# Optimization experiments

Hardware: AMD Instinct MI355X
Metric: run time of the kernel (lower is better)

## Reference

```python
import jax, jax.numpy as jnp
import numpy as np
import math

NUM_SEGMENTS = 4      # num_bezier_segments
SHARPNESS = 75.0
SAMPLE_RATE = 16      # curve samples per bezier segment


def _control_radians(S):
    # replicates the __init__ control-polygon angle construction
    theta = math.pi * 2 / (4 * S) + math.atan(math.tan(2 * math.pi / (4 * S)) / 3.0)
    r = []
    for i in range(S):
        base = 2 * math.pi / S * i
        r += [base, base + theta, 2 * math.pi / S * (i + 1) - theta]
    return jnp.asarray(np.asarray(r, dtype=np.float32).reshape(S, 3))


def _quat_rotate_inv(q, p):
    # rotate p (...,3) by the conjugate of quaternion q (...,4), wxyz convention
    q = q / jnp.linalg.norm(q, axis=-1, keepdims=True)
    w = q[..., 0:1]
    v = -q[..., 1:4]
    t = 2.0 * jnp.cross(v, p)
    return p + w * t + jnp.cross(v, t)


def _csg_stump(points, primitive_parameters, iw, uw, is_training):
    pp = jnp.swapaxes(primitive_parameters, 1, 2)          # (B,K,P)
    B, K, P = pp.shape
    S, R = NUM_SEGMENTS, SAMPLE_RATE
    quat = pp[:, :, :4]
    trans = pp[:, :, 4:7]
    height = pp[:, :, 7]                                   # (B,K)
    radius = jnp.abs(pp[:, :, 8:8 + 3 * S].reshape(B, K, S, 3))
    wts = jnp.abs(pp[:, :, 8 + 3 * S:8 + 5 * S].reshape(B, K, S, 2))

    rad = _control_radians(S)                              # (S,3)
    cp = jnp.stack([jnp.cos(rad) * radius, jnp.sin(rad) * radius], axis=-1)  # (B,K,S,3,2)

    # closed rational cubic bezier spline: segment s uses cp[s,0..2] and cp[s+1,0]
    P0, P1, P2 = cp[:, :, :, 0], cp[:, :, :, 1], cp[:, :, :, 2]
    P3 = jnp.roll(P0, -1, axis=2)
    t = jnp.arange(R, dtype=pp.dtype) / R                  # (R,) endpoint-free
    b0 = (1 - t) ** 3; b1 = 3 * t * (1 - t) ** 2; b2 = 3 * t ** 2 * (1 - t); b3 = t ** 3
    w1 = wts[..., 0:1]; w2 = wts[..., 1:2]                 # (B,K,S,1)
    num = (b0[:, None] * P0[..., None, :]
           + (b1[:, None] * w1[..., None]) * P1[..., None, :]
           + (b2[:, None] * w2[..., None]) * P2[..., None, :]
           + b3[:, None] * P3[..., None, :])               # (B,K,S,R,2)
    den = b0 + b1 * w1 + b2 * w2 + b3                       # (B,K,S,R)
    curve = (num / den[..., None]).reshape(B, K, S * R, 2)  # (B,K,N,2)

    # transform query points into each primitive's local frame
    p_loc = _quat_rotate_inv(quat[:, None], points[:, :, None, :] - trans[:, None])  # (B,M,K,3)
    pxy = p_loc[..., :2]
    pz = p_loc[..., 2]

    # point-to-curve distances without materializing the (B,M,K,N,2) diff
    p_sq = jnp.sum(pxy * pxy, axis=-1)                      # (B,M,K)
    c_sq = jnp.sum(curve * curve, axis=-1)                  # (B,K,N)
    dots = jnp.einsum('bmkd,bknd->bmkn', pxy, curve)
    d = jnp.sqrt(jnp.maximum(p_sq[..., None] + c_sq[:, None] - 2.0 * dots, 0.0) + 1e-12)
    ud = jnp.min(d, axis=-1)                                # (B,M,K) unsigned 2D distance
    idx = jnp.argmin(d, axis=-1)
    curve_r = jnp.sqrt(c_sq)                                # (B,K,N)
    r_near = jnp.take_along_axis(jnp.broadcast_to(curve_r[:, None], d.shape),
                                 idx[..., None], axis=-1)[..., 0]
    sign = jax.lax.stop_gradient(jnp.where(jnp.sqrt(p_sq) <= r_near, -1.0, 1.0))
    sdf2d = sign * ud

    # extrusion along z
    dz = jnp.abs(pz) - height[:, None, :]
    primitive_sdf = (jnp.minimum(jnp.maximum(sdf2d, dz), 0.0)
                     + jnp.sqrt(jnp.maximum(sdf2d, 0.0) ** 2 + jnp.maximum(dz, 0.0) ** 2 + 1e-12))
    support_distances = ud

    occ = jax.nn.sigmoid(-primitive_sdf * SHARPNESS)        # (B,M,K)

    # soft intersection: bkc,bmk->bmkc selection
    pre_i = iw[:, None] * occ[..., None] + (1.0 - iw)[:, None]    # (B,M,K,C)
    if is_training:
        w = jax.lax.stop_gradient(jax.nn.softmax(pre_i * -40.0, axis=-2))
        inter = jnp.sum(w * pre_i, axis=-2)                 # (B,M,C)
    else:
        inter = jnp.min(pre_i, axis=-2)

    # soft union
    pre_u = uw[:, None, :] * inter                          # (B,M,C)
    if is_training:
        w = jax.lax.stop_gradient(jax.nn.softmax(pre_u * 40.0, axis=-1))
        occupancies = jnp.sum(w * pre_u, axis=-1)           # (B,M)
    else:
        occupancies = jnp.max(pre_u, axis=-1)

    return occupancies, primitive_sdf, inter, support_distances


def setup_inputs() -> dict:
    key = jax.random.key(0)
    k1, k2, k3, k4 = jax.random.split(key, 4)
    B, M, K, C = 4, 8192, 64, 32
    P = 8 + 5 * NUM_SEGMENTS  # 28
    return {
        'sample_point_coordinates': jax.random.uniform(k1, (B, M, 3), dtype=jnp.float32),
        'primitive_parameters': jax.random.normal(k2, (B, P, K), dtype=jnp.float32),
        'intersection_layer_weights': jax.random.uniform(k3, (B, K, C), dtype=jnp.float32),
        'union_layer_weights': jax.random.uniform(k4, (B, C), dtype=jnp.float32),
        'is_training': 1,
    }


def reference(sample_point_coordinates, primitive_parameters, intersection_layer_weights,
              union_layer_weights, is_training):
    return _csg_stump(sample_point_coordinates, primitive_parameters,
                      intersection_layer_weights, union_layer_weights, bool(is_training))
```

## Files before the change

### kernel.cpp

```cpp
#include <hip/hip_runtime.h>
#include <math.h>

#define Bb 4
#define Mm 8192
#define Kk 64
#define Cc 32
#define Pp 28

#define OFF_PSDF  (Bb*Mm)
#define OFF_INTER (Bb*Mm + Bb*Mm*Kk)
#define OFF_SD    (Bb*Mm + Bb*Mm*Kk + Bb*Mm*Cc)

#define W40    57.707801635558535f
#define NL2_40 (-0.017328679513998632f)
#define S75    108.20212806667225f
#define EPS_OCC 1e-6f

struct Rad12 { float v[12]; };

__device__ __forceinline__ float fexp2(float x){ return __builtin_amdgcn_exp2f(x); }
__device__ __forceinline__ float frcp(float x){ return __builtin_amdgcn_rcpf(x); }

__global__ __launch_bounds__(256)
void curve_prep(const float* __restrict__ pp, const float* __restrict__ iw_g,
                Rad12 rad,
                float* __restrict__ ws_c, float* __restrict__ ws_cq,
                float* __restrict__ params_ws, float2* __restrict__ st_ws)
{
    const int g = blockIdx.x * 256 + threadIdx.x;
    const int k = g & 63;
    const int n = (g >> 6) & 63;
    const int b = g >> 12;

#define PP(p) pp[((b * Pp) + (p)) * Kk + k]

    const int s  = n >> 4;
    const int it = n & 15;
    const float t = (float)it * 0.0625f;
    const int s1 = (s + 1) & 3;

    float r0 = fabsf(PP(8 + 3 * s + 0));
    float r1 = fabsf(PP(8 + 3 * s + 1));
    float r2 = fabsf(PP(8 + 3 * s + 2));
    float r3 = fabsf(PP(8 + 3 * s1 + 0));
    float w1 = fabsf(PP(20 + 2 * s + 0));
    float w2 = fabsf(PP(20 + 2 * s + 1));

    float a0 = rad.v[3 * s + 0], a1 = rad.v[3 * s + 1];
    float a2 = rad.v[3 * s + 2], a3 = rad.v[3 * s1 + 0];

    float P0x = cosf(a0) * r0, P0y = sinf(a0) * r0;
    float P1x = cosf(a1) * r1, P1y = sinf(a1) * r1;
    float P2x = cosf(a2) * r2, P2y = sinf(a2) * r2;
    float P3x = cosf(a3) * r3, P3y = sinf(a3) * r3;

    float omt = 1.0f - t;
    float b0 = omt * omt * omt;
    float b1 = (3.0f * t) * (omt * omt);
    float b2 = (3.0f * (t * t)) * omt;
    float b3 = t * t * t;
    float bw1 = b1 * w1, bw2 = b2 * w2;
    float den = ((b0 + bw1) + bw2) + b3;
    float nx  = ((b0 * P0x + bw1 * P1x) + bw2 * P2x) + b3 * P3x;
    float ny  = ((b0 * P0y + bw1 * P1y) + bw2 * P2y) + b3 * P3y;

    float cx = nx / den, cy = ny / den;
    const int j = n >> 1, h = n & 1;
    float* base = ws_c + (((b * 32 + j) * 64) + k) * 4;
    base[h]     = -2.0f * cx;
    base[2 + h] = -2.0f * cy;
    ws_cq[(((b * 32 + j) * 64) + k) * 2 + h] = cx * cx + cy * cy;

    if (n < 8) {
        float val;
        if (n < 4) {
            float q0 = PP(0), q1 = PP(1), q2 = PP(2), q3 = PP(3);
            float nrm = sqrtf(q0 * q0 + q1 * q1 + q2 * q2 + q3 * q3);
            val = PP(n) / nrm;
        } else {
            val = PP(n);
        }
        params_ws[(b * Kk + k) * 8 + n] = val;
    }
#undef PP

    if (blockIdx.x == 0 && threadIdx.x < 128) {
        const int tb = threadIdx.x >> 5, tc = threadIdx.x & 31;
        float S = 0.0f, T = 0.0f;
        for (int kk = 0; kk < 64; ++kk) {
            float w   = iw_g[tb * 2048 + kk * 32 + tc];
            float b40 = (w - 1.0f) * W40;
            float e   = fexp2(b40);
            S += e;
            T  = fmaf(e, b40, T);
        }
        st_ws[threadIdx.x] = make_float2(S, T);
    }
}

__global__ __launch_bounds__(512, 6)
void csg_main(const float* __restrict__ pts, const float* __restrict__ iw_g,
              const float* __restrict__ uw_g, const int* __restrict__ flag,
              const float* __restrict__ ws_c, const float* __restrict__ ws_cq,
              const float* __restrict__ params_ws, const float2* __restrict__ st_ws,
              float* __restrict__ out)
{
    __shared__ __align__(16) float s_pool[12352];

    const int tid = threadIdx.x;
    const int bid = blockIdx.x;
    const int b   = bid >> 7;
    const int m0  = (bid & 127) << 6;

    {
        const float4* cs = (const float4*)(ws_c + (size_t)b * 8192);
        float4* cd = (float4*)s_pool;
#pragma unroll
        for (int i = 0; i < 4; ++i) cd[tid + i * 512] = cs[tid + i * 512];
        const float4* qs = (const float4*)(ws_cq + (size_t)b * 4096);
        float4* qd = (float4*)&s_pool[8192];
#pragma unroll
        for (int i = 0; i < 2; ++i) qd[tid + i * 512] = qs[tid + i * 512];
    }
    __syncthreads();

    const int wid  = tid >> 6;
    const int lane = tid & 63;
    const int k    = lane;
    const int pt0  = b * Mm + m0 + (wid << 3);

    const float4* prm4 = (const float4*)(params_ws + ((b << 6) + k) * 8);
    float4 q4 = prm4[0];
    float4 t4 = prm4[1];

    float fl[24];
    {
        const float4* p4 = (const float4*)(pts + (size_t)pt0 * 3);
#pragma unroll
        for (int i = 0; i < 6; ++i) {
            float4 v = p4[i];
            fl[i * 4 + 0] = v.x; fl[i * 4 + 1] = v.y;
            fl[i * 4 + 2] = v.z; fl[i * 4 + 3] = v.w;
        }
    }

    float plx[8], ply[8], plzv[8], psq[8];
    {
        float vx = -q4.y, vy = -q4.z, vz = -q4.w, qw = q4.x;
#pragma unroll
        for (int p = 0; p < 8; ++p) {
            float px = fl[3 * p + 0] - t4.x;
            float py = fl[3 * p + 1] - t4.y;
            float pz = fl[3 * p + 2] - t4.z;
            float t1x = 2.0f * (vy * pz - vz * py);
            float t1y = 2.0f * (vz * px - vx * pz);
            float t1z = 2.0f * (vx * py - vy * px);
            plx[p]  = px + qw * t1x + (vy * t1z - vz * t1y);
            ply[p]  = py + qw * t1y + (vz * t1x - vx * t1z);
            plzv[p] = pz + qw * t1z + (vx * t1y - vy * t1x);
            psq[p]  = plx[p] * plx[p] + ply[p] * ply[p];
        }
    }

    float best[8], bcsq[8];
#pragma unroll
    for (int p = 0; p < 8; ++p) { best[p] = 1e30f; bcsq[p] = 0.0f; }
    {
        const float4* cdp = (const float4*)&s_pool[k * 4];
        const float2* cqp = (const float2*)&s_pool[8192 + k * 2];
#pragma unroll 8
        for (int j = 0; j < 32; ++j) {
            float4 cd  = cdp[j * 64];
            float2 cq2 = cqp[j * 64];
#pragma unroll
            for (int p = 0; p < 8; ++p) {
                float da = fmaf(cd.x, plx[p], fmaf(cd.z, ply[p], cq2.x));
                if (da < best[p]) { best[p] = da; bcsq[p] = cq2.x; }
                float db = fmaf(cd.y, plx[p], fmaf(cd.w, ply[p], cq2.y));
                if (db < best[p]) { best[p] = db; bcsq[p] = cq2.y; }
            }
        }
    }

    float occ[8];
    unsigned long long mask[8];
#pragma unroll
    for (int p = 0; p < 8; ++p) {
        float d2    = psq[p] + best[p];
        float ud    = sqrtf(fmaxf(d2, 0.0f) + 1e-12f);
        float sgn   = (sqrtf(psq[p]) <= sqrtf(bcsq[p])) ? -1.0f : 1.0f;
        float sdf2d = sgn * ud;
        float dzv   = fabsf(plzv[p]) - t4.w;
        float inner = fminf(fmaxf(sdf2d, dzv), 0.0f);
        float r1m   = fmaxf(sdf2d, 0.0f), r2m = fmaxf(dzv, 0.0f);
        float psdf  = inner + sqrtf(r1m * r1m + r2m * r2m + 1e-12f);
        out[OFF_PSDF + (pt0 + p) * Kk + k] = psdf;
        out[OFF_SD   + (pt0 + p) * Kk + k] = ud;
        occ[p]  = frcp(1.0f + fexp2(S75 * psdf));
        mask[p] = __ballot(occ[p] > EPS_OCC);
    }

    __syncthreads();
    {
        const int key  = (k & 15) << 4;
        const int colb = wid << 5;
        char* basep = (char*)s_pool + k * 256;
        *(float4*)(basep + ((colb)      ^ key)) = make_float4(occ[0], occ[1], occ[2], occ[3]);
        *(float4*)(basep + ((colb + 16) ^ key)) = make_float4(occ[4], occ[5], occ[6], occ[7]);
    }
#pragma unroll
    for (int i = 0; i < 4; ++i) {
        int idx = tid + i * 512;
        float w  = iw_g[b * 2048 + idx];
        float a  = w * (-W40);
        float bb = (w - 1.0f) * W40;
        float e0 = fexp2(bb);
        ((float2*)&s_pool[4096])[idx] = make_float2(a, bb);
        ((float2*)&s_pool[8192])[idx] = make_float2(e0, e0 * bb);
    }
    if (tid < 32) ((float2*)&s_pool[12288])[tid] = st_ws[b * 32 + tid];
    __syncthreads();

    const int training = flag[0];
    const int c = lane & 31;
    const float2* wvt = (const float2*)&s_pool[4096];
    const float2* e0t = (const float2*)&s_pool[8192];

    float inter[8];
    if (training) {
        float2 s0t0 = ((const float2*)&s_pool[12288])[c];
#pragma unroll
        for (int p = 0; p < 8; ++p) {
            unsigned long long m = mask[p];
            const int pt4 = ((wid << 3) + p) << 2;
            float sw = s0t0.x, swp = s0t0.y;
            while (m) {
                int kk = __builtin_ctzll(m); m &= m - 1;
                float osv = *(const float*)((const char*)s_pool +
                              kk * 256 + (pt4 ^ ((kk & 15) << 4)));
                float2 wv = wvt[kk * 32 + c];
                float2 e0 = e0t[kk * 32 + c];
                float pre = fmaf(wv.x, osv, wv.y);
                float e   = fexp2(pre);
                sw  += (e - e0.x);
                swp += fmaf(e, pre, -e0.y);
            }
            inter[p] = swp * frcp(sw) * NL2_40;
        }
    } else {
        const int kb = lane & 32;
#pragma unroll
        for (int p = 0; p < 8; ++p) {
            const int pt4 = ((wid << 3) + p) << 2;
            float mx = -1e30f;
            for (int j = 0; j < 32; ++j) {
                int row = kb + j;
                float osv = *(const float*)((const char*)s_pool +
                              row * 256 + (pt4 ^ ((row & 15) << 4)));
                float2 wv = wvt[row * 32 + c];
                mx = fmaxf(mx, fmaf(wv.x, osv, wv.y));
            }
            mx = fmaxf(mx, __shfl_xor(mx, 32, 64));
            inter[p] = mx * NL2_40;
        }
    }

    if (lane < Cc) {
#pragma unroll
        for (int p = 0; p < 8; ++p)
            out[OFF_INTER + (pt0 + p) * Cc + c] = inter[p];
    }

    float uwv = uw_g[b * Cc + c];
    float resv[8];
    if (training) {
#pragma unroll
        for (int p = 0; p < 8; ++p) {
            float pu  = uwv * inter[p];
            float e   = fexp2(W40 * pu);
            float num = e * pu, den = e;
#pragma unroll
            for (int msk = 16; msk >= 1; msk >>= 1) {
                num += __shfl_xor(num, msk, 64);
                den += __shfl_xor(den, msk, 64);
            }
            resv[p] = num * frcp(den);
        }
    } else {
#pragma unroll
        for (int p = 0; p < 8; ++p) {
            float pu = uwv * inter[p];
#pragma unroll
            for (int msk = 16; msk >= 1; msk >>= 1)
                pu = fmaxf(pu, __shfl_xor(pu, msk, 64));
            resv[p] = pu;
        }
    }
    if (lane == 0) {
        *(float4*)(out + pt0)     = make_float4(resv[0], resv[1], resv[2], resv[3]);
        *(float4*)(out + pt0 + 4) = make_float4(resv[4], resv[5], resv[6], resv[7]);
    }
}

extern "C" void kernel_launch(void* const* d_in, const int* in_sizes, int n_in,
                              void* d_out, int out_size, void* d_ws, size_t ws_size,
                              hipStream_t stream)
{
    const float* pts  = (const float*)d_in[0];
    const float* pp   = (const float*)d_in[1];
    const float* iw   = (const float*)d_in[2];
    const float* uw   = (const float*)d_in[3];
    const int*   flag = (const int*)d_in[4];
    float* out = (float*)d_out;

    float*  ws_c   = (float*)d_ws;
    float*  ws_cq  = ws_c + 32768;
    float*  params = ws_cq + 16384;
    float2* st_ws  = (float2*)(params + 2048);

    Rad12 rad;
    const double th = M_PI * 2.0 / 16.0 + atan(tan(2.0 * M_PI / 16.0) / 3.0);
    for (int i = 0; i < 4; ++i) {
        double base = 2.0 * M_PI / 4.0 * (double)i;
        rad.v[3 * i + 0] = (float)base;
        rad.v[3 * i + 1] = (float)(base + th);
        rad.v[3 * i + 2] = (float)(2.0 * M_PI / 4.0 * (double)(i + 1) - th);
    }

    curve_prep<<<64, 256, 0, stream>>>(pp, iw, rad, ws_c, ws_cq, params, st_ws);
    csg_main<<<Bb * Mm / 64, 512, 0, stream>>>(pts, iw, uw, flag,
                                               ws_c, ws_cq, params, st_ws, out);
}
```

Before: 42.52 us.

## Halve points per wave and merge LDS weight tables into one float4 table

Each wave now processes 4 points instead of 8, which doubles the grid to 1024 blocks of 32 points and relaxes the occupancy hint from 6 to 4. The occupancy staging in shared memory becomes a plain point-major layout instead of a swizzled k-major one. The two float2 weight tables are merged into a single float4 table so the inner loop does one LDS load per k. The aim is more parallelism and fewer LDS instructions, at the cost of reloading the curve table into LDS for twice as many blocks and possible bank conflicts from the unswizzled layout.

Measured after the change: 42.92 us. About the same (+0.9%).

```diff
diff --git a/kernel.cpp b/kernel.cpp
--- a/kernel.cpp
+++ b/kernel.cpp
@@ -98,7 +98,7 @@
     }
 }
 
-__global__ __launch_bounds__(512, 6)
+__global__ __launch_bounds__(512, 4)
 void csg_main(const float* __restrict__ pts, const float* __restrict__ iw_g,
               const float* __restrict__ uw_g, const int* __restrict__ flag,
               const float* __restrict__ ws_c, const float* __restrict__ ws_cq,
@@ -109,8 +109,8 @@
 
     const int tid = threadIdx.x;
     const int bid = blockIdx.x;
-    const int b   = bid >> 7;
-    const int m0  = (bid & 127) << 6;
+    const int b   = bid >> 8;
+    const int m0  = (bid & 255) << 5;
 
     {
         const float4* cs = (const float4*)(ws_c + (size_t)b * 8192);
@@ -127,31 +127,24 @@
     const int wid  = tid >> 6;
     const int lane = tid & 63;
     const int k    = lane;
-    const int pt0  = b * Mm + m0 + (wid << 3);
+    const int pt0  = b * Mm + m0 + (wid << 2);
 
     const float4* prm4 = (const float4*)(params_ws + ((b << 6) + k) * 8);
     float4 q4 = prm4[0];
     float4 t4 = prm4[1];
 
-    float fl[24];
-    {
-        const float4* p4 = (const float4*)(pts + (size_t)pt0 * 3);
-#pragma unroll
-        for (int i = 0; i < 6; ++i) {
-            float4 v = p4[i];
-            fl[i * 4 + 0] = v.x; fl[i * 4 + 1] = v.y;
-            fl[i * 4 + 2] = v.z; fl[i * 4 + 3] = v.w;
-        }
-    }
-
-    float plx[8], ply[8], plzv[8], psq[8];
+    const float4* pts4 = (const float4*)(pts + (size_t)pt0 * 3);
+    float4 A = pts4[0], Bv = pts4[1], Cv = pts4[2];
+    float pxs[4] = {A.x, A.w, Bv.z, Cv.y};
+    float pys[4] = {A.y, Bv.x, Bv.w, Cv.z};
+    float pzs[4] = {A.z, Bv.y, Cv.x, Cv.w};
+
+    float plx[4], ply[4], plzv[4], psq[4];
     {
         float vx = -q4.y, vy = -q4.z, vz = -q4.w, qw = q4.x;
 #pragma unroll
-        for (int p = 0; p < 8; ++p) {
-            float px = fl[3 * p + 0] - t4.x;
-            float py = fl[3 * p + 1] - t4.y;
-            float pz = fl[3 * p + 2] - t4.z;
+        for (int p = 0; p < 4; ++p) {
+            float px = pxs[p] - t4.x, py = pys[p] - t4.y, pz = pzs[p] - t4.z;
             float t1x = 2.0f * (vy * pz - vz * py);
             float t1y = 2.0f * (vz * px - vx * pz);
             float t1z = 2.0f * (vx * py - vy * px);
@@ -162,18 +155,17 @@
         }
     }
 
-    float best[8], bcsq[8];
-#pragma unroll
-    for (int p = 0; p < 8; ++p) { best[p] = 1e30f; bcsq[p] = 0.0f; }
+    float best[4] = {1e30f, 1e30f, 1e30f, 1e30f};
+    float bcsq[4] = {0.0f, 0.0f, 0.0f, 0.0f};
     {
         const float4* cdp = (const float4*)&s_pool[k * 4];
         const float2* cqp = (const float2*)&s_pool[8192 + k * 2];
-#pragma unroll 8
+#pragma unroll
         for (int j = 0; j < 32; ++j) {
             float4 cd  = cdp[j * 64];
             float2 cq2 = cqp[j * 64];
 #pragma unroll
-            for (int p = 0; p < 8; ++p) {
+            for (int p = 0; p < 4; ++p) {
                 float da = fmaf(cd.x, plx[p], fmaf(cd.z, ply[p], cq2.x));
                 if (da < best[p]) { best[p] = da; bcsq[p] = cq2.x; }
                 float db = fmaf(cd.y, plx[p], fmaf(cd.w, ply[p], cq2.y));
@@ -182,10 +174,10 @@
         }
     }
 
-    float occ[8];
-    unsigned long long mask[8];
-#pragma unroll
-    for (int p = 0; p < 8; ++p) {
+    float occ[4];
+    unsigned long long mask[4];
+#pragma unroll
+    for (int p = 0; p < 4; ++p) {
         float d2    = psq[p] + best[p];
         float ud    = sqrtf(fmaxf(d2, 0.0f) + 1e-12f);
         float sgn   = (sqrtf(psq[p]) <= sqrtf(bcsq[p])) ? -1.0f : 1.0f;
@@ -202,11 +194,10 @@
 
     __syncthreads();
     {
-        const int key  = (k & 15) << 4;
-        const int colb = wid << 5;
-        char* basep = (char*)s_pool + k * 256;
-        *(float4*)(basep + ((colb)      ^ key)) = make_float4(occ[0], occ[1], occ[2], occ[3]);
-        *(float4*)(basep + ((colb + 16) ^ key)) = make_float4(occ[4], occ[5], occ[6], occ[7]);
+        const int ptl = wid << 2;
+#pragma unroll
+        for (int p = 0; p < 4; ++p)
+            s_pool[(ptl + p) * 64 + k] = occ[p];
     }
 #pragma unroll
     for (int i = 0; i < 4; ++i) {
@@ -215,67 +206,59 @@
         float a  = w * (-W40);
         float bb = (w - 1.0f) * W40;
         float e0 = fexp2(bb);
-        ((float2*)&s_pool[4096])[idx] = make_float2(a, bb);
-        ((float2*)&s_pool[8192])[idx] = make_float2(e0, e0 * bb);
+        ((float4*)&s_pool[2048])[idx] = make_float4(a, bb, e0, e0 * bb);
     }
     if (tid < 32) ((float2*)&s_pool[12288])[tid] = st_ws[b * 32 + tid];
     __syncthreads();
 
     const int training = flag[0];
     const int c = lane & 31;
-    const float2* wvt = (const float2*)&s_pool[4096];
-    const float2* e0t = (const float2*)&s_pool[8192];
-
-    float inter[8];
+    const float4* tbl = (const float4*)&s_pool[2048];
+
+    float inter[4];
     if (training) {
         float2 s0t0 = ((const float2*)&s_pool[12288])[c];
 #pragma unroll
-        for (int p = 0; p < 8; ++p) {
+        for (int p = 0; p < 4; ++p) {
             unsigned long long m = mask[p];
-            const int pt4 = ((wid << 3) + p) << 2;
+            const int ptl = (wid << 2) + p;
             float sw = s0t0.x, swp = s0t0.y;
             while (m) {
                 int kk = __builtin_ctzll(m); m &= m - 1;
-                float osv = *(const float*)((const char*)s_pool +
-                              kk * 256 + (pt4 ^ ((kk & 15) << 4)));
-                float2 wv = wvt[kk * 32 + c];
-                float2 e0 = e0t[kk * 32 + c];
+                float osv = s_pool[ptl * 64 + kk];
+                float4 wv = tbl[kk * 32 + c];
                 float pre = fmaf(wv.x, osv, wv.y);
                 float e   = fexp2(pre);
-                sw  += (e - e0.x);
-                swp += fmaf(e, pre, -e0.y);
+                sw  += (e - wv.z);
+                swp += fmaf(e, pre, -wv.w);
             }
             inter[p] = swp * frcp(sw) * NL2_40;
         }
     } else {
-        const int kb = lane & 32;
-#pragma unroll
-        for (int p = 0; p < 8; ++p) {
-            const int pt4 = ((wid << 3) + p) << 2;
+#pragma unroll
+        for (int p = 0; p < 4; ++p) {
+            const int ptl = (wid << 2) + p;
             float mx = -1e30f;
-            for (int j = 0; j < 32; ++j) {
-                int row = kb + j;
-                float osv = *(const float*)((const char*)s_pool +
-                              row * 256 + (pt4 ^ ((row & 15) << 4)));
-                float2 wv = wvt[row * 32 + c];
+            for (int kk = 0; kk < 64; ++kk) {
+                float osv = s_pool[ptl * 64 + kk];
+                float4 wv = tbl[kk * 32 + c];
                 mx = fmaxf(mx, fmaf(wv.x, osv, wv.y));
             }
-            mx = fmaxf(mx, __shfl_xor(mx, 32, 64));
             inter[p] = mx * NL2_40;
         }
     }
 
     if (lane < Cc) {
 #pragma unroll
-        for (int p = 0; p < 8; ++p)
+        for (int p = 0; p < 4; ++p)
             out[OFF_INTER + (pt0 + p) * Cc + c] = inter[p];
     }
 
     float uwv = uw_g[b * Cc + c];
-    float resv[8];
+    float resv[4];
     if (training) {
 #pragma unroll
-        for (int p = 0; p < 8; ++p) {
+        for (int p = 0; p < 4; ++p) {
             float pu  = uwv * inter[p];
             float e   = fexp2(W40 * pu);
             float num = e * pu, den = e;
@@ -288,7 +271,7 @@
         }
     } else {
 #pragma unroll
-        for (int p = 0; p < 8; ++p) {
+        for (int p = 0; p < 4; ++p) {
             float pu = uwv * inter[p];
 #pragma unroll
             for (int msk = 16; msk >= 1; msk >>= 1)
@@ -296,10 +279,8 @@
             resv[p] = pu;
         }
     }
-    if (lane == 0) {
-        *(float4*)(out + pt0)     = make_float4(resv[0], resv[1], resv[2], resv[3]);
-        *(float4*)(out + pt0 + 4) = make_float4(resv[4], resv[5], resv[6], resv[7]);
-    }
+    if (lane == 0)
+        *(float4*)(out + pt0) = make_float4(resv[0], resv[1], resv[2], resv[3]);
 }
 
 extern "C" void kernel_launch(void* const* d_in, const int* in_sizes, int n_in,
@@ -328,6 +309,6 @@
     }
 
     curve_prep<<<64, 256, 0, stream>>>(pp, iw, rad, ws_c, ws_cq, params, st_ws);
-    csg_main<<<Bb * Mm / 64, 512, 0, stream>>>(pts, iw, uw, flag,
+    csg_main<<<Bb * Mm / 32, 512, 0, stream>>>(pts, iw, uw, flag,
                                                ws_c, ws_cq, params, st_ws, out);
 }
```
